# Optimization experiments

Measured on AMD Instinct MI355X. Metric: run time of the kernel, lower is better.

## Reference

```python
import jax, jax.numpy as jnp
import numpy as np

KERNEL_SIZE = 3  # matches init kwarg

def setup_inputs() -> dict:
    key = jax.random.key(0)
    k1, k2, k3, k4 = jax.random.split(key, 4)
    N, C, L, OUT = 32, 64, 2048, 128
    inp = jax.random.normal(k1, (N, C, L), dtype=jnp.float32)
    # adjacency-like dense matrix (tree adjacency may be sparse; dense here)
    m = jax.random.uniform(k2, (N, L, L), dtype=jnp.float32)
    W = jax.random.normal(k3, (OUT, KERNEL_SIZE * C), dtype=jnp.float32) * 0.05
    b = jax.random.normal(k4, (OUT,), dtype=jnp.float32)
    return {"input": inp, "m": m, "W": W, "b": b}

def reference(input, m, W, b):
    # propagate features over the tree adjacency kernel_size-1 times
    ys = [input]
    y = input
    for _ in range(KERNEL_SIZE - 1):
        y = jnp.matmul(y, m)          # (N, C, L) @ (N, L, L) -> (N, C, L)
        ys.append(y)
    cat = jnp.concatenate(ys, axis=1)  # (N, k*C, L)
    # 1x1 conv == channel projection
    out = jnp.einsum('oc,ncl->nol', W, cat) + b[None, :, None]
    return out
```

## Files before the change

### kernel.cpp

```cpp
#include <hip/hip_runtime.h>
#include <hip/hip_bf16.h>

#define NB   32
#define CH   64
#define LL   2048
#define OUTC 128

typedef float  f32x4  __attribute__((ext_vector_type(4)));
typedef short  s16x8  __attribute__((ext_vector_type(8)));
typedef unsigned short u16;

__device__ __forceinline__ u16 f2bf(float f) {
  unsigned int u = __builtin_bit_cast(unsigned int, f);
  u += 0x7FFFu + ((u >> 16) & 1u);
  return (u16)(u >> 16);
}

__device__ __forceinline__ s16x8 pack8c(const float* v) {
  s16x8 r;
#pragma unroll
  for (int j = 0; j < 8; j += 2) {
    __hip_bfloat162 h = __float22bfloat162_rn(make_float2(v[j], v[j + 1]));
    short2 s;
    __builtin_memcpy(&s, &h, sizeof(s));
    r[j] = s.x; r[j + 1] = s.y;
  }
  return r;
}

#define NX (NB * CH * LL)
#define NW (OUTC * 3 * CH)
__global__ __launch_bounds__(256)
void cvt_inputs(const float* __restrict__ x, const float* __restrict__ W,
                u16* __restrict__ xb, u16* __restrict__ Wb)
{
  const size_t t8 = ((size_t)blockIdx.x * 256 + threadIdx.x) * 8;
  if (t8 < NX) {
    float v[8];
    *(f32x4*)(v)     = *(const f32x4*)(x + t8);
    *(f32x4*)(v + 4) = *(const f32x4*)(x + t8 + 4);
    *(s16x8*)(xb + t8) = pack8c(v);
  } else if (t8 - NX < NW) {
    const size_t w8 = t8 - NX;
    float v[8];
    *(f32x4*)(v)     = *(const f32x4*)(W + w8);
    *(f32x4*)(v + 4) = *(const f32x4*)(W + w8 + 4);
    *(s16x8*)(Wb + w8) = pack8c(v);
  }
}

__global__ __launch_bounds__(256, 2)
void prop1_pack(const u16* __restrict__ xb, const float* __restrict__ m,
                u16* __restrict__ y1, u16* __restrict__ mP)
{
  __shared__ float smem[2][32 * 128];

  const int n    = blockIdx.x >> 4;
  const int lt   = blockIdx.x & 15;
  const int tid  = threadIdx.x;
  const int wave = tid >> 6;
  const int lane = tid & 63;
  const int l15  = lane & 15;
  const int g4   = lane >> 4;
  const int colb = lt * 128 + wave * 32;

  const float* mn = m  + (size_t)n * LL * LL + lt * 128;
  const u16*   ap = xb + (size_t)n * CH * LL + (size_t)l15 * LL + g4 * 8;
  u16* q0 = mP + (((size_t)n * 64 * LL + colb + l15) * 4 + g4) * 8;
  u16* o  = y1 + (size_t)n * CH * LL + colb + l15;

  f32x4 acc[4][2];
#pragma unroll
  for (int f = 0; f < 4; ++f)
#pragma unroll
    for (int h = 0; h < 2; ++h)
#pragma unroll
      for (int r = 0; r < 4; ++r) acc[f][h][r] = 0.f;

  f32x4 rg[4];

#define LOADR(KB)                                                            \
  { _Pragma("unroll") for (int i = 0; i < 4; ++i) {                          \
      const int _od = (tid + 256 * i) * 4;                                   \
      rg[i] = *(const f32x4*)(mn + (size_t)((KB) * 32 + (_od >> 7)) * LL +   \
                              (_od & 127)); } }

  LOADR(0)
#pragma unroll 1
  for (int kb = 0; kb < 64; ++kb) {
    {
      float* s = smem[kb & 1];
#pragma unroll
      for (int i = 0; i < 4; ++i)
        *(f32x4*)(s + (size_t)(tid + 256 * i) * 4) = rg[i];
    }
    if (kb < 63) LOADR(kb + 1)
    __syncthreads();

    const float* t = smem[kb & 1] + wave * 32 + l15;
    float bv0[8], bv1[8];
#pragma unroll
    for (int j = 0; j < 8; ++j) {
      bv0[j] = t[(g4 * 8 + j) * 128];
      bv1[j] = t[(g4 * 8 + j) * 128 + 16];
    }
    s16x8 b0 = pack8c(bv0), b1 = pack8c(bv1);

    u16* q = q0 + (size_t)kb * 65536;
    *(s16x8*)(q)       = b0;
    *(s16x8*)(q + 512) = b1;

    const u16* a_ = ap + kb * 32;
#pragma unroll
    for (int f = 0; f < 4; ++f) {
      s16x8 af = *(const s16x8*)(a_ + (size_t)(f * 16) * LL);
      acc[f][0] = __builtin_amdgcn_mfma_f32_16x16x32_bf16(af, b0, acc[f][0], 0, 0, 0);
      acc[f][1] = __builtin_amdgcn_mfma_f32_16x16x32_bf16(af, b1, acc[f][1], 0, 0, 0);
    }
  }

#pragma unroll
  for (int f = 0; f < 4; ++f)
#pragma unroll
    for (int r = 0; r < 4; ++r) {
      const int row = f * 16 + g4 * 4 + r;
      o[(size_t)row * LL]      = f2bf(acc[f][0][r]);
      o[(size_t)row * LL + 16] = f2bf(acc[f][1][r]);
    }
}

__global__ __launch_bounds__(256, 2)
void prop2(const u16* __restrict__ y1, const u16* __restrict__ mP,
           u16* __restrict__ y2)
{
  const int n    = blockIdx.x >> 4;
  const int lt   = blockIdx.x & 15;
  const int tid  = threadIdx.x;
  const int wave = tid >> 6;
  const int lane = tid & 63;
  const int l15  = lane & 15;
  const int g4   = lane >> 4;
  const int colb = lt * 128 + wave * 32;

  const u16* mq = mP + (((size_t)n * 64 * LL + colb + l15) * 4 + g4) * 8;
  const u16* ap = y1 + (size_t)n * CH * LL + (size_t)l15 * LL + g4 * 8;
  u16* o = y2 + (size_t)n * CH * LL + colb + l15;

  f32x4 acc[4][2];
#pragma unroll
  for (int f = 0; f < 4; ++f)
#pragma unroll
    for (int h = 0; h < 2; ++h)
#pragma unroll
      for (int r = 0; r < 4; ++r) acc[f][h][r] = 0.f;

  s16x8 bA0, bA1, bB0, bB1, aA[4], aB[4];

#define K2_LOAD(B0, B1, AV, KB)                                              \
  {                                                                          \
    const u16* _mq = mq + (size_t)(KB) * 65536;                              \
    B0 = *(const s16x8*)(_mq);                                               \
    B1 = *(const s16x8*)(_mq + 512);                                         \
    const u16* _ap = ap + (KB) * 32;                                         \
    _Pragma("unroll") for (int f = 0; f < 4; ++f)                            \
      AV[f] = *(const s16x8*)(_ap + (size_t)(f * 16) * LL);                  \
  }

#define K2_COMP(B0, B1, AV)                                                  \
  _Pragma("unroll") for (int f = 0; f < 4; ++f) {                            \
    acc[f][0] = __builtin_amdgcn_mfma_f32_16x16x32_bf16(AV[f], B0, acc[f][0], 0, 0, 0); \
    acc[f][1] = __builtin_amdgcn_mfma_f32_16x16x32_bf16(AV[f], B1, acc[f][1], 0, 0, 0); \
  }

  K2_LOAD(bA0, bA1, aA, 0)
#pragma unroll 1
  for (int kb = 0; kb < 64; kb += 2) {
    K2_LOAD(bB0, bB1, aB, kb + 1)
    K2_COMP(bA0, bA1, aA)
    if (kb + 2 < 64) K2_LOAD(bA0, bA1, aA, kb + 2)
    K2_COMP(bB0, bB1, aB)
  }

#pragma unroll
  for (int f = 0; f < 4; ++f)
#pragma unroll
    for (int r = 0; r < 4; ++r) {
      const int row = f * 16 + g4 * 4 + r;
      o[(size_t)row * LL]      = f2bf(acc[f][0][r]);
      o[(size_t)row * LL + 16] = f2bf(acc[f][1][r]);
    }
}

__global__ __launch_bounds__(256)
void proj(const u16* __restrict__ xb, const u16* __restrict__ y1,
          const u16* __restrict__ y2, const u16* __restrict__ Wb,
          const float* __restrict__ bias, float* __restrict__ out)
{
  const int n    = blockIdx.x >> 4;
  const int lt   = blockIdx.x & 15;
  const int tid  = threadIdx.x;
  const int wave = tid >> 6;
  const int lane = tid & 63;
  const int l15  = lane & 15;
  const int g4   = lane >> 4;
  const int colb = lt * 128 + wave * 32;

  f32x4 acc[8][2];
#pragma unroll
  for (int f = 0; f < 8; ++f)
#pragma unroll
    for (int h = 0; h < 2; ++h)
#pragma unroll
      for (int r = 0; r < 4; ++r) acc[f][h][r] = 0.f;

  const size_t cb = (size_t)n * CH * LL + colb + l15;
  const u16* xp  = xb + cb + (size_t)(g4 * 8) * LL;
  const u16* y1p = y1 + cb + (size_t)(g4 * 8) * LL;
  const u16* y2p = y2 + cb + (size_t)(g4 * 8) * LL;
  const u16* wq  = Wb + (size_t)l15 * 192 + g4 * 8;

#pragma unroll
  for (int kc = 0; kc < 6; ++kc) {
    const int k0 = kc * 32;
    s16x8 b0, b1;
    const u16* src = (k0 < 64) ? (xp + (size_t)k0 * LL)
                   : (k0 < 128) ? (y1p + (size_t)(k0 - 64) * LL)
                                : (y2p + (size_t)(k0 - 128) * LL);
#pragma unroll
    for (int j = 0; j < 8; ++j) {
      b0[j] = (short)src[(size_t)j * LL];
      b1[j] = (short)src[(size_t)j * LL + 16];
    }

#pragma unroll
    for (int f = 0; f < 8; ++f) {
      s16x8 af = *(const s16x8*)(wq + (size_t)(f * 16) * 192 + k0);
      acc[f][0] = __builtin_amdgcn_mfma_f32_16x16x32_bf16(af, b0, acc[f][0], 0, 0, 0);
      acc[f][1] = __builtin_amdgcn_mfma_f32_16x16x32_bf16(af, b1, acc[f][1], 0, 0, 0);
    }
  }

  float* op = out + (size_t)n * OUTC * LL + colb + l15;
#pragma unroll
  for (int f = 0; f < 8; ++f)
#pragma unroll
    for (int r = 0; r < 4; ++r) {
      const int row = f * 16 + g4 * 4 + r;
      op[(size_t)row * LL]      = acc[f][0][r] + bias[row];
      op[(size_t)row * LL + 16] = acc[f][1][r] + bias[row];
    }
}

extern "C" void kernel_launch(void* const* d_in, const int* in_sizes, int n_in,
                              void* d_out, int out_size, void* d_ws, size_t ws_size,
                              hipStream_t stream)
{
  const float* x = (const float*)d_in[0];
  const float* m = (const float*)d_in[1];
  const float* W = (const float*)d_in[2];
  const float* b = (const float*)d_in[3];
  float* out = (float*)d_out;

  u16* y1 = (u16*)d_ws;
  u16* y2 = y1 + (size_t)NB * CH * LL;
  u16* xb = y2 + (size_t)NB * CH * LL;
  u16* Wb = xb + (size_t)NB * CH * LL;
  u16* mP = (u16*)((char*)d_ws + (25u << 20));

  cvt_inputs<<<dim3(2060), dim3(256), 0, stream>>>(x, W, xb, Wb);
  prop1_pack<<<dim3(NB * 16), dim3(256), 0, stream>>>(xb, m, y1, mP);
  prop2<<<dim3(NB * 16), dim3(256), 0, stream>>>(y1, mP, y2);
  proj<<<dim3(NB * 16), dim3(256), 0, stream>>>(xb, y1, y2, Wb, b, out);
}
```

Measured before the change: 284.4 us.

## Stream m tiles via direct global-to-LDS loads and fuse prop2 with projection

prop1_pack now loads m tiles straight into LDS with global_load_lds, using a triple-buffered ring with vmcnt waits and barriers instead of staging through registers. This is meant to keep more loads in flight and cut register and LDS write traffic. prop2 and proj are merged into one kernel: the y2 tile is kept in LDS (transposed, padded) and fed directly into the projection, which removes the y2 global write and read and one launch. The cost is more LDS per block and hand-written waitcnt synchronization that has to be correct.

```diff
diff --git a/kernel.cpp b/kernel.cpp
--- a/kernel.cpp
+++ b/kernel.cpp
@@ -8,6 +8,7 @@
 
 typedef float  f32x4  __attribute__((ext_vector_type(4)));
 typedef short  s16x8  __attribute__((ext_vector_type(8)));
+typedef short  s16x4  __attribute__((ext_vector_type(4)));
 typedef unsigned short u16;
 
 __device__ __forceinline__ u16 f2bf(float f) {
@@ -25,6 +26,17 @@
     __builtin_memcpy(&s, &h, sizeof(s));
     r[j] = s.x; r[j + 1] = s.y;
   }
+  return r;
+}
+
+__device__ __forceinline__ s16x4 pack4c(const f32x4& v) {
+  s16x4 r;
+  __hip_bfloat162 h0 = __float22bfloat162_rn(make_float2(v[0], v[1]));
+  __hip_bfloat162 h1 = __float22bfloat162_rn(make_float2(v[2], v[3]));
+  short2 s0, s1;
+  __builtin_memcpy(&s0, &h0, sizeof(s0));
+  __builtin_memcpy(&s1, &h1, sizeof(s1));
+  r[0] = s0.x; r[1] = s0.y; r[2] = s1.x; r[3] = s1.y;
   return r;
 }
 
@@ -53,7 +65,7 @@
 void prop1_pack(const u16* __restrict__ xb, const float* __restrict__ m,
                 u16* __restrict__ y1, u16* __restrict__ mP)
 {
-  __shared__ float smem[2][32 * 128];
+  __shared__ float smem[3][32 * 128];
 
   const int n    = blockIdx.x >> 4;
   const int lt   = blockIdx.x & 15;
@@ -64,8 +76,10 @@
   const int g4   = lane >> 4;
   const int colb = lt * 128 + wave * 32;
 
-  const float* mn = m  + (size_t)n * LL * LL + lt * 128;
-  const u16*   ap = xb + (size_t)n * CH * LL + (size_t)l15 * LL + g4 * 8;
+  const float* mn = m + (size_t)n * LL * LL + lt * 128;
+  const float* gsrc = mn + (size_t)(wave * 8 + (lane >> 5)) * LL + (lane & 31) * 4;
+
+  const u16* ap = xb + (size_t)n * CH * LL + (size_t)l15 * LL + g4 * 8;
   u16* q0 = mP + (((size_t)n * 64 * LL + colb + l15) * 4 + g4) * 8;
   u16* o  = y1 + (size_t)n * CH * LL + colb + l15;
 
@@ -77,27 +91,34 @@
 #pragma unroll
       for (int r = 0; r < 4; ++r) acc[f][h][r] = 0.f;
 
-  f32x4 rg[4];
-
-#define LOADR(KB)                                                            \
-  { _Pragma("unroll") for (int i = 0; i < 4; ++i) {                          \
-      const int _od = (tid + 256 * i) * 4;                                   \
-      rg[i] = *(const f32x4*)(mn + (size_t)((KB) * 32 + (_od >> 7)) * LL +   \
-                              (_od & 127)); } }
-
-  LOADR(0)
+#define GLOAD(SB, KB)                                                         \
+  { float* _sb = (SB);                                                        \
+    _Pragma("unroll") for (int i = 0; i < 4; ++i) {                           \
+      const float* _g = gsrc + (size_t)((KB) * 32 + i * 2) * LL;              \
+      __builtin_amdgcn_global_load_lds(                                       \
+        (const __attribute__((address_space(1))) void*)_g,                    \
+        (__attribute__((address_space(3))) void*)(_sb + (wave * 4 + i) * 256),\
+        16, 0, 0); } }
+
+  GLOAD(smem[0], 0)
+  GLOAD(smem[1], 1)
+  asm volatile("s_waitcnt vmcnt(4)" ::: "memory");
+  __builtin_amdgcn_s_barrier();
+  __builtin_amdgcn_sched_barrier(0);
+
+  int bc = 0;
 #pragma unroll 1
   for (int kb = 0; kb < 64; ++kb) {
-    {
-      float* s = smem[kb & 1];
-#pragma unroll
-      for (int i = 0; i < 4; ++i)
-        *(f32x4*)(s + (size_t)(tid + 256 * i) * 4) = rg[i];
-    }
-    if (kb < 63) LOADR(kb + 1)
-    __syncthreads();
-
-    const float* t = smem[kb & 1] + wave * 32 + l15;
+    s16x8 a[4];
+    const u16* a_ = ap + kb * 32;
+#pragma unroll
+    for (int f = 0; f < 4; ++f) a[f] = *(const s16x8*)(a_ + (size_t)(f * 16) * LL);
+    __builtin_amdgcn_sched_barrier(0);
+
+    const int b2 = (bc == 0) ? 2 : bc - 1;
+    if (kb + 2 < 64) GLOAD(smem[b2], kb + 2)
+
+    const float* t = smem[bc] + wave * 32 + l15;
     float bv0[8], bv1[8];
 #pragma unroll
     for (int j = 0; j < 8; ++j) {
@@ -110,13 +131,18 @@
     *(s16x8*)(q)       = b0;
     *(s16x8*)(q + 512) = b1;
 
-    const u16* a_ = ap + kb * 32;
 #pragma unroll
     for (int f = 0; f < 4; ++f) {
-      s16x8 af = *(const s16x8*)(a_ + (size_t)(f * 16) * LL);
-      acc[f][0] = __builtin_amdgcn_mfma_f32_16x16x32_bf16(af, b0, acc[f][0], 0, 0, 0);
-      acc[f][1] = __builtin_amdgcn_mfma_f32_16x16x32_bf16(af, b1, acc[f][1], 0, 0, 0);
-    }
+      acc[f][0] = __builtin_amdgcn_mfma_f32_16x16x32_bf16(a[f], b0, acc[f][0], 0, 0, 0);
+      acc[f][1] = __builtin_amdgcn_mfma_f32_16x16x32_bf16(a[f], b1, acc[f][1], 0, 0, 0);
+    }
+
+    if (kb + 1 < 64) {
+      asm volatile("s_waitcnt vmcnt(6)" ::: "memory");
+      __builtin_amdgcn_s_barrier();
+      __builtin_amdgcn_sched_barrier(0);
+    }
+    bc = (bc == 2) ? 0 : bc + 1;
   }
 
 #pragma unroll
@@ -130,9 +156,12 @@
 }
 
 __global__ __launch_bounds__(256, 2)
-void prop2(const u16* __restrict__ y1, const u16* __restrict__ mP,
-           u16* __restrict__ y2)
-{
+void prop2_proj(const u16* __restrict__ y1, const u16* __restrict__ mP,
+                const u16* __restrict__ xb, const u16* __restrict__ Wb,
+                const float* __restrict__ bias, float* __restrict__ out)
+{
+  __shared__ u16 yT[128 * 72];
+
   const int n    = blockIdx.x >> 4;
   const int lt   = blockIdx.x & 15;
   const int tid  = threadIdx.x;
@@ -144,7 +173,6 @@
 
   const u16* mq = mP + (((size_t)n * 64 * LL + colb + l15) * 4 + g4) * 8;
   const u16* ap = y1 + (size_t)n * CH * LL + (size_t)l15 * LL + g4 * 8;
-  u16* o = y2 + (size_t)n * CH * LL + colb + l15;
 
   f32x4 acc[4][2];
 #pragma unroll
@@ -184,59 +212,47 @@
 #pragma unroll
   for (int f = 0; f < 4; ++f)
 #pragma unroll
-    for (int r = 0; r < 4; ++r) {
-      const int row = f * 16 + g4 * 4 + r;
-      o[(size_t)row * LL]      = f2bf(acc[f][0][r]);
-      o[(size_t)row * LL + 16] = f2bf(acc[f][1][r]);
-    }
-}
-
-__global__ __launch_bounds__(256)
-void proj(const u16* __restrict__ xb, const u16* __restrict__ y1,
-          const u16* __restrict__ y2, const u16* __restrict__ Wb,
-          const float* __restrict__ bias, float* __restrict__ out)
-{
-  const int n    = blockIdx.x >> 4;
-  const int lt   = blockIdx.x & 15;
-  const int tid  = threadIdx.x;
-  const int wave = tid >> 6;
-  const int lane = tid & 63;
-  const int l15  = lane & 15;
-  const int g4   = lane >> 4;
-  const int colb = lt * 128 + wave * 32;
-
-  f32x4 acc[8][2];
+    for (int h = 0; h < 2; ++h) {
+      const int c = wave * 32 + l15 + 16 * h;
+      *(s16x4*)(&yT[c * 72 + f * 16 + g4 * 4]) = pack4c(acc[f][h]);
+    }
+  __syncthreads();
+
+  f32x4 acc2[8][2];
 #pragma unroll
   for (int f = 0; f < 8; ++f)
 #pragma unroll
     for (int h = 0; h < 2; ++h)
 #pragma unroll
-      for (int r = 0; r < 4; ++r) acc[f][h][r] = 0.f;
+      for (int r = 0; r < 4; ++r) acc2[f][h][r] = 0.f;
 
   const size_t cb = (size_t)n * CH * LL + colb + l15;
   const u16* xp  = xb + cb + (size_t)(g4 * 8) * LL;
   const u16* y1p = y1 + cb + (size_t)(g4 * 8) * LL;
-  const u16* y2p = y2 + cb + (size_t)(g4 * 8) * LL;
   const u16* wq  = Wb + (size_t)l15 * 192 + g4 * 8;
 
 #pragma unroll
   for (int kc = 0; kc < 6; ++kc) {
     const int k0 = kc * 32;
     s16x8 b0, b1;
-    const u16* src = (k0 < 64) ? (xp + (size_t)k0 * LL)
-                   : (k0 < 128) ? (y1p + (size_t)(k0 - 64) * LL)
-                                : (y2p + (size_t)(k0 - 128) * LL);
-#pragma unroll
-    for (int j = 0; j < 8; ++j) {
-      b0[j] = (short)src[(size_t)j * LL];
-      b1[j] = (short)src[(size_t)j * LL + 16];
-    }
-
+    if (kc < 4) {
+      const u16* src = (kc < 2) ? (xp + (size_t)k0 * LL)
+                                : (y1p + (size_t)(k0 - 64) * LL);
+#pragma unroll
+      for (int j = 0; j < 8; ++j) {
+        b0[j] = (short)src[(size_t)j * LL];
+        b1[j] = (short)src[(size_t)j * LL + 16];
+      }
+    } else {
+      const int rb = (kc - 4) * 32 + g4 * 8;
+      b0 = *(const s16x8*)(&yT[(wave * 32 + l15) * 72 + rb]);
+      b1 = *(const s16x8*)(&yT[(wave * 32 + l15 + 16) * 72 + rb]);
+    }
 #pragma unroll
     for (int f = 0; f < 8; ++f) {
       s16x8 af = *(const s16x8*)(wq + (size_t)(f * 16) * 192 + k0);
-      acc[f][0] = __builtin_amdgcn_mfma_f32_16x16x32_bf16(af, b0, acc[f][0], 0, 0, 0);
-      acc[f][1] = __builtin_amdgcn_mfma_f32_16x16x32_bf16(af, b1, acc[f][1], 0, 0, 0);
+      acc2[f][0] = __builtin_amdgcn_mfma_f32_16x16x32_bf16(af, b0, acc2[f][0], 0, 0, 0);
+      acc2[f][1] = __builtin_amdgcn_mfma_f32_16x16x32_bf16(af, b1, acc2[f][1], 0, 0, 0);
     }
   }
 
@@ -246,8 +262,8 @@
 #pragma unroll
     for (int r = 0; r < 4; ++r) {
       const int row = f * 16 + g4 * 4 + r;
-      op[(size_t)row * LL]      = acc[f][0][r] + bias[row];
-      op[(size_t)row * LL + 16] = acc[f][1][r] + bias[row];
+      op[(size_t)row * LL]      = acc2[f][0][r] + bias[row];
+      op[(size_t)row * LL + 16] = acc2[f][1][r] + bias[row];
     }
 }
 
@@ -262,13 +278,11 @@
   float* out = (float*)d_out;
 
   u16* y1 = (u16*)d_ws;
-  u16* y2 = y1 + (size_t)NB * CH * LL;
-  u16* xb = y2 + (size_t)NB * CH * LL;
+  u16* xb = y1 + (size_t)NB * CH * LL;
   u16* Wb = xb + (size_t)NB * CH * LL;
   u16* mP = (u16*)((char*)d_ws + (25u << 20));
 
   cvt_inputs<<<dim3(2060), dim3(256), 0, stream>>>(x, W, xb, Wb);
   prop1_pack<<<dim3(NB * 16), dim3(256), 0, stream>>>(xb, m, y1, mP);
-  prop2<<<dim3(NB * 16), dim3(256), 0, stream>>>(y1, mP, y2);
-  proj<<<dim3(NB * 16), dim3(256), 0, stream>>>(xb, y1, y2, Wb, b, out);
-}
+  prop2_proj<<<dim3(NB * 16), dim3(256), 0, stream>>>(y1, mP, xb, Wb, b, out);
+}
```

Result: no change. 279.6 us (-1.7%).
